# Kernel tuning notes

Measured on AMD Instinct MI355X. Metric: run time of the kernel, lower is better.

## Reference

```python
import jax, jax.numpy as jnp
import numpy as np

B, C, D, W, H = 4, 256, 32, 32, 32  # img_dim = D, in_channels = C, model_num = 4


def setup_inputs() -> dict:
    key = jax.random.key(0)
    ks = jax.random.split(key, 8)
    s = 0.02
    inp = {
        "m1": jax.random.normal(ks[0], (B, C, D, W, H), jnp.float32),
        "m2": jax.random.normal(ks[1], (B, C, D, W, H), jnp.float32),
        "m3": jax.random.normal(ks[2], (B, C, D, W, H), jnp.float32),
        "m4": jax.random.normal(ks[3], (B, C, D, W, H), jnp.float32),
        # nn.Linear weights (torch convention: y = x @ W.T + b)
        "Wq": jax.random.normal(ks[4], (D, D), jnp.float32) * s,
        "bq": jnp.zeros((D,), jnp.float32),
        "Wk": jax.random.normal(ks[5], (D, D), jnp.float32) * s,
        "bk": jnp.zeros((D,), jnp.float32),
        # four 1x1x1 Conv3d kernels, squeezed to [model, out_c, in_c]
        "Wc": jax.random.normal(ks[6], (4, C, C), jnp.float32) * s,
        "bc": jnp.zeros((4, C), jnp.float32),
    }
    return inp


def reference(m1, m2, m3, m4, Wq, bq, Wk, bk, Wc, bc):
    d = m1.shape[2]
    # adaptive_avg_pool3d(x, (D,1,1)) == mean over W,H -> [B,C,D]; stack 4 modalities -> [B,C,4,D]
    pooled = jnp.stack([m.mean(axis=(3, 4)) for m in (m1, m2, m3, m4)], axis=2)
    q = jnp.einsum('bcd,ed->bce', pooled[:, :, 0], Wq) + bq          # [B,C,D]
    k = jnp.einsum('bcmd,ed->bcme', pooled, Wk) + bk                 # [B,C,4,D]
    # per-modality attention logits: q . k_m over D -> [B,C,4]
    a = jnp.einsum('bcd,bcmd->bcm', q, k) / jnp.sqrt(jnp.float32(d))
    a = jax.nn.softmax(a, axis=-1)                                   # [B,C,4]
    ms = jnp.stack([m1, m2, m3, m4], axis=0)                         # [4,B,C,D,W,H]
    # 1x1x1 Conv3d == channel-mixing GEMM per voxel
    conv = jnp.einsum('mbcdwh,moc->mbodwh', ms, Wc) + bc[:, None, :, None, None, None]
    # weighted sum of the 4 conv outputs by per-(B,C) attention weights
    out = jnp.einsum('bcm,mbcdwh->bcdwh', a, conv)                   # [B,C,D,W,H]
    return out
```

## Files before the change

kernel.cpp:

```cpp
#include <hip/hip_runtime.h>
#include <hip/hip_bf16.h>

#define NB 4
#define NC 256
#define ND 32
#define WH 1024
#define DWH 32768
#define KTOT 1024

typedef __attribute__((ext_vector_type(8))) short short8;
typedef __attribute__((ext_vector_type(4))) float f32x4;

static __device__ __forceinline__ unsigned short f32_to_bf16(float f) {
    unsigned u = __builtin_bit_cast(unsigned, f);
    u = u + 0x7fff + ((u >> 16) & 1);
    return (unsigned short)(u >> 16);
}

static __device__ __forceinline__ unsigned pack_bf16x2(float lo, float hi) {
    __hip_bfloat162 h = __float22bfloat162_rn(make_float2(lo, hi));
    unsigned u;
    __builtin_memcpy(&u, &h, 4);
    return u;
}

__global__ __launch_bounds__(256) void transpool_kernel(
    const float* __restrict__ i0, const float* __restrict__ i1,
    const float* __restrict__ i2, const float* __restrict__ i3,
    unsigned short* __restrict__ Bt, float* __restrict__ pooled)
{
    __shared__ float lds[8 * 1024];
    int raw = blockIdx.x;
    int sb  = (raw & 7) * 2048 + (raw >> 3);
    int d    = sb & 31;
    int cb8  = (sb >> 5) & 31;
    int m    = (sb >> 10) & 3;
    int b    = sb >> 12;
    const float* base = (m == 0 ? i0 : m == 1 ? i1 : m == 2 ? i2 : i3)
                        + ((size_t)(b * NC + cb8 * 8)) * DWH + d * WH;

    int t = threadIdx.x;
    int row    = t >> 5;
    int lane32 = t & 31;

    float4 v[8];
    #pragma unroll
    for (int j = 0; j < 8; ++j)
        v[j] = *(const float4*)(base + (size_t)row * DWH + lane32 * 4 + j * 128);

    float s = 0.f;
    #pragma unroll
    for (int j = 0; j < 8; ++j)
        s += (v[j].x + v[j].y) + (v[j].z + v[j].w);

    #pragma unroll
    for (int j = 0; j < 8; ++j)
        *(float4*)&lds[row * 1024 + lane32 * 4 + j * 128] = v[j];
    __syncthreads();

    float4 c0 = *(const float4*)&lds[0 * 1024 + 4 * t];
    float4 c1 = *(const float4*)&lds[1 * 1024 + 4 * t];
    float4 c2 = *(const float4*)&lds[2 * 1024 + 4 * t];
    float4 c3 = *(const float4*)&lds[3 * 1024 + 4 * t];
    float4 c4 = *(const float4*)&lds[4 * 1024 + 4 * t];
    float4 c5 = *(const float4*)&lds[5 * 1024 + 4 * t];
    float4 c6 = *(const float4*)&lds[6 * 1024 + 4 * t];
    float4 c7 = *(const float4*)&lds[7 * 1024 + 4 * t];

    int kt = m * 4 + (cb8 >> 3);
    int kc = cb8 & 7;
    unsigned short* dst = Bt
        + ((((size_t)b * 16 + kt) * 8 + kc) * 32768 + (size_t)d * 1024 + 4 * t) * 8;
    const float* f0 = (const float*)&c0;  const float* f1 = (const float*)&c1;
    const float* f2 = (const float*)&c2;  const float* f3 = (const float*)&c3;
    const float* f4 = (const float*)&c4;  const float* f5 = (const float*)&c5;
    const float* f6 = (const float*)&c6;  const float* f7 = (const float*)&c7;
    #pragma unroll
    for (int xi = 0; xi < 4; ++xi) {
        uint4 pk = (uint4){pack_bf16x2(f0[xi], f1[xi]),
                           pack_bf16x2(f2[xi], f3[xi]),
                           pack_bf16x2(f4[xi], f5[xi]),
                           pack_bf16x2(f6[xi], f7[xi])};
        *(uint4*)(dst + xi * 8) = pk;
    }

    s += __shfl_down(s, 16, 64);
    s += __shfl_down(s, 8, 64);
    s += __shfl_down(s, 4, 64);
    s += __shfl_down(s, 2, 64);
    s += __shfl_down(s, 1, 64);
    if (lane32 == 0) {
        int c = cb8 * 8 + row;
        pooled[((size_t)b * NC + c) * 128 + m * 32 + d] = s * (1.0f / 1024.0f);
    }
}

__global__ __launch_bounds__(256) void pool_kernel(
    const float* __restrict__ i0, const float* __restrict__ i1,
    const float* __restrict__ i2, const float* __restrict__ i3,
    float* __restrict__ pooled)
{
    int bid = blockIdx.x;
    int m   = bid & 3;
    int bc  = bid >> 2;
    const float* src = (m == 0 ? i0 : m == 1 ? i1 : m == 2 ? i2 : i3)
                       + (size_t)bc * DWH;
    int t = threadIdx.x;
    int d   = t >> 3;
    int sub = t & 7;

    const float4* row = (const float4*)(src + (size_t)d * WH);
    float4 a0 = {0.f, 0.f, 0.f, 0.f}, a1 = {0.f, 0.f, 0.f, 0.f};
    #pragma unroll
    for (int j = 0; j < 16; ++j) {
        float4 u = row[sub + 8 * (2 * j)];
        float4 w = row[sub + 8 * (2 * j + 1)];
        a0.x += u.x; a0.y += u.y; a0.z += u.z; a0.w += u.w;
        a1.x += w.x; a1.y += w.y; a1.z += w.z; a1.w += w.w;
    }
    float s = (a0.x + a0.y) + (a0.z + a0.w) + (a1.x + a1.y) + (a1.z + a1.w);
    s += __shfl_down(s, 4, 64);
    s += __shfl_down(s, 2, 64);
    s += __shfl_down(s, 1, 64);
    if (sub == 0) pooled[bc * 128 + m * 32 + d] = s * (1.0f / 1024.0f);
}

__global__ __launch_bounds__(64) void attn_kernel(
    const float* __restrict__ pooled,
    const float* __restrict__ Wq, const float* __restrict__ bq,
    const float* __restrict__ Wk, const float* __restrict__ bk,
    const float* __restrict__ Wc, const float* __restrict__ bcv,
    unsigned short* __restrict__ Amat, float* __restrict__ beff)
{
    int bc_idx = blockIdx.x;
    int lane = threadIdx.x;
    int e = lane & 31;
    const float* P = pooled + bc_idx * 128;

    float q = 0.f, kv[4] = {0.f, 0.f, 0.f, 0.f};
    for (int d = 0; d < 32; ++d) {
        float pq = P[d];
        float wq = Wq[e * 32 + d], wk = Wk[e * 32 + d];
        q += pq * wq;
        #pragma unroll
        for (int m = 0; m < 4; ++m) kv[m] += P[m * 32 + d] * wk;
    }
    q += bq[e];
    #pragma unroll
    for (int m = 0; m < 4; ++m) kv[m] += bk[e];

    float lg[4];
    #pragma unroll
    for (int m = 0; m < 4; ++m) {
        float p = q * kv[m];
        #pragma unroll
        for (int off = 16; off; off >>= 1) p += __shfl_xor(p, off, 32);
        lg[m] = p * 0.17677669529663687f;
    }
    float mx = fmaxf(fmaxf(lg[0], lg[1]), fmaxf(lg[2], lg[3]));
    float ex[4], s = 0.f;
    #pragma unroll
    for (int m = 0; m < 4; ++m) { ex[m] = __expf(lg[m] - mx); s += ex[m]; }
    float a[4];
    #pragma unroll
    for (int m = 0; m < 4; ++m) a[m] = ex[m] / s;

    int c = bc_idx & 255;
    if (lane == 0) {
        float be = 0.f;
        #pragma unroll
        for (int m = 0; m < 4; ++m) be += a[m] * bcv[m * NC + c];
        beff[bc_idx] = be;
    }
    unsigned short* Arow = Amat + (size_t)bc_idx * KTOT;
    #pragma unroll
    for (int j = 0; j < 16; ++j) {
        int k = j * 64 + lane;
        int m = k >> 8, cin = k & 255;
        float v = a[m] * Wc[(m * NC + c) * NC + cin];
        Arow[k] = f32_to_bf16(v);
    }
}

#define BM 128
#define BN 128
#define BK 64

static __device__ __forceinline__ int swzA(int row, int chunk) {
    return row * 64 + ((chunk ^ (row & 7)) << 3);
}
static __device__ __forceinline__ int swzB(int row, int chunk) {
    return row * 64 + ((chunk ^ ((row >> 1) & 7)) << 3);
}

__global__ __launch_bounds__(256, 2) void gemm2_kernel(
    const unsigned short* __restrict__ Amat,
    const unsigned short* __restrict__ Bt,
    const float* __restrict__ beff,
    float* __restrict__ out)
{
    __shared__ __align__(16) short As[2 * BM * BK];
    __shared__ __align__(16) short Bs[2 * BN * BK];

    int raw = blockIdx.x;
    int sb  = (raw & 7) * 256 + (raw >> 3);
    int ot = sb & 1;
    int xt = (sb >> 1) & 255;
    int b  = sb >> 9;
    int o0 = ot * BM, x0 = xt * BN;

    int t = threadIdx.x;
    int wave = t >> 6, lane = t & 63;
    int wr = wave >> 1, wc = wave & 1;
    int lrow = lane & 15, lk = lane >> 4;
    int lr8 = lane >> 3;
    int aq  = (lane & 7) ^ lr8;

    const unsigned short* asrc = Amat + ((size_t)b * NC + o0) * KTOT
                                 + (size_t)(wave * 32 + lr8) * KTOT + aq * 8;
    const unsigned short* bsrc = Bt + (size_t)b * 16 * 2097152
                                 + (size_t)aq * 262144
                                 + ((size_t)xt * 128 + wave * 32 + lr8) * 8;

    f32x4 acc[4][4];
    #pragma unroll
    for (int mi = 0; mi < 4; ++mi)
        #pragma unroll
        for (int ni = 0; ni < 4; ++ni)
            acc[mi][ni] = (f32x4){0.f, 0.f, 0.f, 0.f};

    #pragma unroll
    for (int p = 0; p < 4; ++p)
        __builtin_amdgcn_global_load_lds(
            (const __attribute__((address_space(1))) unsigned int*)
                (asrc + (size_t)p * 8 * KTOT),
            (__attribute__((address_space(3))) unsigned int*)
                (As + (wave * 32 + p * 8) * 64), 16, 0, 0);
    #pragma unroll
    for (int p = 0; p < 4; ++p)
        __builtin_amdgcn_global_load_lds(
            (const __attribute__((address_space(1))) unsigned int*)
                (bsrc + (size_t)p * 64),
            (__attribute__((address_space(3))) unsigned int*)
                (Bs + (wave * 32 + p * 8) * 64), 16, 0, 0);
    __builtin_amdgcn_sched_barrier(0);

    #pragma unroll 1
    for (int it = 0; it < 16; ++it) {
        int ja = (it < 15) ? it + 1 : 15;
        int bo = ((it + 1) & 1) * (BM * BK);
        #pragma unroll
        for (int p = 0; p < 4; ++p)
            __builtin_amdgcn_global_load_lds(
                (const __attribute__((address_space(1))) unsigned int*)
                    (asrc + (size_t)p * 8 * KTOT + ja * BK),
                (__attribute__((address_space(3))) unsigned int*)
                    (As + bo + (wave * 32 + p * 8) * 64), 16, 0, 0);
        #pragma unroll
        for (int p = 0; p < 4; ++p)
            __builtin_amdgcn_global_load_lds(
                (const __attribute__((address_space(1))) unsigned int*)
                    (bsrc + (size_t)ja * 2097152 + p * 64),
                (__attribute__((address_space(3))) unsigned int*)
                    (Bs + bo + (wave * 32 + p * 8) * 64), 16, 0, 0);
        __builtin_amdgcn_sched_barrier(0);

        asm volatile("s_waitcnt vmcnt(8)" ::: "memory");
        __builtin_amdgcn_s_barrier();
        __builtin_amdgcn_sched_barrier(0);

        const short* Acur = As + (it & 1) * (BM * BK);
        const short* Bcur = Bs + (it & 1) * (BM * BK);
        #pragma unroll
        for (int kk = 0; kk < 2; ++kk) {
            int q = kk * 4 + lk;
            short8 af[4], bf[4];
            #pragma unroll
            for (int mi = 0; mi < 4; ++mi)
                af[mi] = *(const short8*)(&Acur[swzA(wr * 64 + mi * 16 + lrow, q)]);
            #pragma unroll
            for (int ni = 0; ni < 4; ++ni)
                bf[ni] = *(const short8*)(&Bcur[swzA(wc * 64 + ni * 16 + lrow, q)]);
            __builtin_amdgcn_s_setprio(1);
            #pragma unroll
            for (int mi = 0; mi < 4; ++mi)
                #pragma unroll
                for (int ni = 0; ni < 4; ++ni)
                    acc[mi][ni] = __builtin_amdgcn_mfma_f32_16x16x32_bf16(
                        af[mi], bf[ni], acc[mi][ni], 0, 0, 0);
            __builtin_amdgcn_s_setprio(0);
        }
        __builtin_amdgcn_s_barrier();
        __builtin_amdgcn_sched_barrier(0);
    }

    const float* beff_b = beff + b * NC + o0;
    float* outb = out + ((size_t)b * NC + o0) * DWH + x0;
    #pragma unroll
    for (int mi = 0; mi < 4; ++mi) {
        #pragma unroll
        for (int r4 = 0; r4 < 4; ++r4) {
            int row = wr * 64 + mi * 16 + lk * 4 + r4;
            float bias = beff_b[row];
            float* orow = outb + (size_t)row * DWH;
            #pragma unroll
            for (int ni = 0; ni < 4; ++ni) {
                int col = wc * 64 + ni * 16 + lrow;
                orow[col] = acc[mi][ni][r4] + bias;
            }
        }
    }
}

__global__ __launch_bounds__(256, 3) void gemm_kernel(
    const float* __restrict__ i0, const float* __restrict__ i1,
    const float* __restrict__ i2, const float* __restrict__ i3,
    const unsigned short* __restrict__ Amat,
    const float* __restrict__ beff,
    float* __restrict__ out)
{
    __shared__ __align__(16) short As[2 * BM * BK];
    __shared__ __align__(16) short Bs[BN * BK];

    int raw = blockIdx.x;
    int sb  = (raw & 7) * 256 + (raw >> 3);
    int ot = sb & 1;
    int xt = (sb >> 1) & 255;
    int b  = sb >> 9;
    int o0 = ot * BM, x0 = xt * BN;

    const unsigned short* Ab = Amat + ((size_t)b * NC + o0) * KTOT;

    int t = threadIdx.x;
    int wave = t >> 6, lane = t & 63;
    int wr = wave >> 1, wc = wave & 1;
    int lrow = lane & 15, lk = lane >> 4;

    f32x4 acc[4][4];
    #pragma unroll
    for (int mi = 0; mi < 4; ++mi)
        #pragma unroll
        for (int ni = 0; ni < 4; ++ni)
            acc[mi][ni] = (f32x4){0.f, 0.f, 0.f, 0.f};

    int xq = t & 31;
    int kb = (t >> 5) * 8;

    int ar = wave * 32 + (lane >> 3);
    int aq = (lane & 7) ^ (lane >> 3);
    const unsigned short* asrc = Ab + (size_t)ar * KTOT + aq * 8;

    float4 v[8];

    {
        #pragma unroll
        for (int p = 0; p < 4; ++p)
            __builtin_amdgcn_global_load_lds(
                (const __attribute__((address_space(1))) unsigned int*)
                    (asrc + (size_t)p * 8 * KTOT),
                (__attribute__((address_space(3))) unsigned int*)
                    (As + (wave * 32 + p * 8) * 64), 16, 0, 0);
        const float* Bb = i0 + (size_t)b * NC * DWH + x0;
        #pragma unroll
        for (int j = 0; j < 8; ++j)
            v[j] = *(const float4*)(Bb + (size_t)(kb + j) * DWH + xq * 4);
    }

    #pragma unroll 1
    for (int it = 0; it < KTOT / BK; ++it) {
        const short* Acur = As + (it & 1) * (BM * BK);
        short* Anx = As + ((it + 1) & 1) * (BM * BK);

        __builtin_amdgcn_s_barrier();
        __builtin_amdgcn_sched_barrier(0);

        {
            int ja = (it + 1 < 16) ? it + 1 : 15;
            #pragma unroll
            for (int p = 0; p < 4; ++p)
                __builtin_amdgcn_global_load_lds(
                    (const __attribute__((address_space(1))) unsigned int*)
                        (asrc + (size_t)p * 8 * KTOT + ja * BK),
                    (__attribute__((address_space(3))) unsigned int*)
                        (Anx + (wave * 32 + p * 8) * 64), 16, 0, 0);
        }
        __builtin_amdgcn_sched_barrier(0);

        uint4 pk[4];
        #pragma unroll
        for (int i = 0; i < 4; ++i) {
            unsigned w[4];
            #pragma unroll
            for (int j = 0; j < 4; ++j)
                w[j] = pack_bf16x2(((const float*)&v[2 * j])[i],
                                   ((const float*)&v[2 * j + 1])[i]);
            pk[i] = (uint4){w[0], w[1], w[2], w[3]};
        }

        {
            int itn = (it < 15) ? it + 1 : 15;
            int m = itn >> 2, cbase = (itn & 3) * 64;
            const float* Bb = (m == 0 ? i0 : m == 1 ? i1 : m == 2 ? i2 : i3)
                              + ((size_t)b * NC + cbase) * DWH + x0;
            #pragma unroll
            for (int j = 0; j < 8; ++j)
                v[j] = *(const float4*)(Bb + (size_t)(kb + j) * DWH + xq * 4);
        }
        __builtin_amdgcn_sched_barrier(0);

        #pragma unroll
        for (int i = 0; i < 4; ++i)
            *(uint4*)(&Bs[swzB(xq * 4 + i, t >> 5)]) = pk[i];

        asm volatile("s_waitcnt vmcnt(12) lgkmcnt(0)" ::: "memory");
        __builtin_amdgcn_s_barrier();
        __builtin_amdgcn_sched_barrier(0);

        #pragma unroll
        for (int kk = 0; kk < 2; ++kk) {
            int q = kk * 4 + lk;
            short8 af[4], bf[4];
            #pragma unroll
            for (int mi = 0; mi < 4; ++mi)
                af[mi] = *(const short8*)(&Acur[swzA(wr * 64 + mi * 16 + lrow, q)]);
            #pragma unroll
            for (int ni = 0; ni < 4; ++ni)
                bf[ni] = *(const short8*)(&Bs[swzB(wc * 64 + ni * 16 + lrow, q)]);
            __builtin_amdgcn_s_setprio(1);
            #pragma unroll
            for (int mi = 0; mi < 4; ++mi)
                #pragma unroll
                for (int ni = 0; ni < 4; ++ni)
                    acc[mi][ni] = __builtin_amdgcn_mfma_f32_16x16x32_bf16(
                        af[mi], bf[ni], acc[mi][ni], 0, 0, 0);
            __builtin_amdgcn_s_setprio(0);
        }
    }

    const float* beff_b = beff + b * NC + o0;
    float* outb = out + ((size_t)b * NC + o0) * DWH + x0;
    #pragma unroll
    for (int mi = 0; mi < 4; ++mi) {
        #pragma unroll
        for (int r4 = 0; r4 < 4; ++r4) {
            int row = wr * 64 + mi * 16 + lk * 4 + r4;
            float bias = beff_b[row];
            float* orow = outb + (size_t)row * DWH;
            #pragma unroll
            for (int ni = 0; ni < 4; ++ni) {
                int col = wc * 64 + ni * 16 + lrow;
                orow[col] = acc[mi][ni][r4] + bias;
            }
        }
    }
}

extern "C" void kernel_launch(void* const* d_in, const int* in_sizes, int n_in,
                              void* d_out, int out_size, void* d_ws, size_t ws_size,
                              hipStream_t stream) {
    const float* m1 = (const float*)d_in[0];
    const float* m2 = (const float*)d_in[1];
    const float* m3 = (const float*)d_in[2];
    const float* m4 = (const float*)d_in[3];
    const float* Wq = (const float*)d_in[4];
    const float* bq = (const float*)d_in[5];
    const float* Wk = (const float*)d_in[6];
    const float* bk = (const float*)d_in[7];
    const float* Wc = (const float*)d_in[8];
    const float* bcv = (const float*)d_in[9];
    float* out = (float*)d_out;

    const size_t BT_BYTES = (size_t)NB * KTOT * DWH * 2;
    const size_t NEED = BT_BYTES + 524288 + 2097152 + 4096;

    if (ws_size >= NEED) {
        unsigned short* Btr   = (unsigned short*)d_ws;
        float* pooled         = (float*)((char*)d_ws + BT_BYTES);
        unsigned short* Amat  = (unsigned short*)((char*)d_ws + BT_BYTES + 524288);
        float* beff           = (float*)((char*)d_ws + BT_BYTES + 524288 + 2097152);

        transpool_kernel<<<16384, 256, 0, stream>>>(m1, m2, m3, m4, Btr, pooled);
        attn_kernel<<<NB * NC, 64, 0, stream>>>(pooled, Wq, bq, Wk, bk, Wc, bcv,
                                                Amat, beff);
        gemm2_kernel<<<2048, 256, 0, stream>>>(Amat, Btr, beff, out);
    } else {
        float* pooled        = (float*)d_ws;
        unsigned short* Amat = (unsigned short*)((char*)d_ws + 524288);
        float* beff          = (float*)((char*)d_ws + 524288 + 2097152);

        pool_kernel<<<NB * NC * 4, 256, 0, stream>>>(m1, m2, m3, m4, pooled);
        attn_kernel<<<NB * NC, 64, 0, stream>>>(pooled, Wq, bq, Wk, bk, Wc, bcv,
                                                Amat, beff);
        gemm_kernel<<<(NB) * (NC / BM) * (DWH / BN), 256, 0, stream>>>(
            m1, m2, m3, m4, Amat, beff, out);
    }
}
```

Before: 294.9 us.

## Make transpose-pool kernel persistent over 8 depth slices with register double buffering

The transpose/pool kernel now has each block process 8 consecutive depth slices instead of one, and the grid shrinks from 16384 to 2048 blocks. Loads for the next slice go into a second register buffer while the current slice is written through LDS, converted to bf16 and stored, so global reads overlap the LDS transpose. This is meant to hide memory latency and cut per-block launch overhead. It roughly doubles register use, which may lower occupancy, and adds two barriers per slice.

New measurement: 305.0 us. 3.4% more time.

```diff
diff --git a/kernel.cpp b/kernel.cpp
--- a/kernel.cpp
+++ b/kernel.cpp
@@ -23,6 +23,55 @@
     __builtin_memcpy(&u, &h, 4);
     return u;
 }
+
+#define TP_LOAD(V, J)                                                         \
+  { const float* bs_ = base + (size_t)(J) * WH;                               \
+    _Pragma("unroll")                                                         \
+    for (int j_ = 0; j_ < 8; ++j_)                                            \
+      V[j_] = *(const float4*)(bs_ + (size_t)row * DWH + lane32 * 4 + j_ * 128); }
+
+#define TP_ITEM(VC, VN, J)                                                    \
+  {                                                                           \
+    _Pragma("unroll")                                                         \
+    for (int j_ = 0; j_ < 8; ++j_)                                            \
+      *(float4*)&lds[row * 1024 + lane32 * 4 + j_ * 128] = VC[j_];            \
+    if ((J) + 1 < 8) { TP_LOAD(VN, (J) + 1); }                                \
+    asm volatile("s_waitcnt lgkmcnt(0)" ::: "memory");                        \
+    __builtin_amdgcn_s_barrier();                                             \
+    __builtin_amdgcn_sched_barrier(0);                                        \
+    {                                                                         \
+      float4 c_[8];                                                           \
+      _Pragma("unroll")                                                       \
+      for (int ci_ = 0; ci_ < 8; ++ci_)                                       \
+        c_[ci_] = *(const float4*)&lds[ci_ * 1024 + 4 * t];                   \
+      unsigned short* dst_ = dstbase + (size_t)(d0 + (J)) * 8192 + (size_t)t * 32; \
+      _Pragma("unroll")                                                       \
+      for (int xi_ = 0; xi_ < 4; ++xi_) {                                     \
+        uint4 pk_ = (uint4){                                                  \
+          pack_bf16x2(((const float*)&c_[0])[xi_], ((const float*)&c_[1])[xi_]), \
+          pack_bf16x2(((const float*)&c_[2])[xi_], ((const float*)&c_[3])[xi_]), \
+          pack_bf16x2(((const float*)&c_[4])[xi_], ((const float*)&c_[5])[xi_]), \
+          pack_bf16x2(((const float*)&c_[6])[xi_], ((const float*)&c_[7])[xi_])};\
+        *(uint4*)(dst_ + xi_ * 8) = pk_;                                      \
+      }                                                                       \
+    }                                                                         \
+    {                                                                         \
+      float s_ = 0.f;                                                         \
+      _Pragma("unroll")                                                       \
+      for (int j_ = 0; j_ < 8; ++j_)                                          \
+        s_ += (VC[j_].x + VC[j_].y) + (VC[j_].z + VC[j_].w);                  \
+      s_ += __shfl_down(s_, 16, 64);                                          \
+      s_ += __shfl_down(s_, 8, 64);                                           \
+      s_ += __shfl_down(s_, 4, 64);                                           \
+      s_ += __shfl_down(s_, 2, 64);                                           \
+      s_ += __shfl_down(s_, 1, 64);                                           \
+      if (lane32 == 0)                                                        \
+        pooled[((size_t)b * NC + cb8 * 8 + row) * 128 + m * 32 + d0 + (J)]    \
+            = s_ * (1.0f / 1024.0f);                                          \
+    }                                                                         \
+    __builtin_amdgcn_s_barrier();                                             \
+    __builtin_amdgcn_sched_barrier(0);                                        \
+  }
 
 __global__ __launch_bounds__(256) void transpool_kernel(
     const float* __restrict__ i0, const float* __restrict__ i1,
@@ -31,67 +80,29 @@
 {
     __shared__ float lds[8 * 1024];
     int raw = blockIdx.x;
-    int sb  = (raw & 7) * 2048 + (raw >> 3);
-    int d    = sb & 31;
-    int cb8  = (sb >> 5) & 31;
-    int m    = (sb >> 10) & 3;
-    int b    = sb >> 12;
+    int sp  = (raw & 7) * 256 + (raw >> 3);
+    int d0   = (sp & 3) * 8;
+    int cb8  = (sp >> 2) & 31;
+    int m    = (sp >> 7) & 3;
+    int b    = sp >> 9;
     const float* base = (m == 0 ? i0 : m == 1 ? i1 : m == 2 ? i2 : i3)
-                        + ((size_t)(b * NC + cb8 * 8)) * DWH + d * WH;
+                        + ((size_t)(b * NC + cb8 * 8)) * DWH + d0 * WH;
 
     int t = threadIdx.x;
     int row    = t >> 5;
     int lane32 = t & 31;
 
-    float4 v[8];
-    #pragma unroll
-    for (int j = 0; j < 8; ++j)
-        v[j] = *(const float4*)(base + (size_t)row * DWH + lane32 * 4 + j * 128);
-
-    float s = 0.f;
-    #pragma unroll
-    for (int j = 0; j < 8; ++j)
-        s += (v[j].x + v[j].y) + (v[j].z + v[j].w);
-
-    #pragma unroll
-    for (int j = 0; j < 8; ++j)
-        *(float4*)&lds[row * 1024 + lane32 * 4 + j * 128] = v[j];
-    __syncthreads();
-
-    float4 c0 = *(const float4*)&lds[0 * 1024 + 4 * t];
-    float4 c1 = *(const float4*)&lds[1 * 1024 + 4 * t];
-    float4 c2 = *(const float4*)&lds[2 * 1024 + 4 * t];
-    float4 c3 = *(const float4*)&lds[3 * 1024 + 4 * t];
-    float4 c4 = *(const float4*)&lds[4 * 1024 + 4 * t];
-    float4 c5 = *(const float4*)&lds[5 * 1024 + 4 * t];
-    float4 c6 = *(const float4*)&lds[6 * 1024 + 4 * t];
-    float4 c7 = *(const float4*)&lds[7 * 1024 + 4 * t];
-
     int kt = m * 4 + (cb8 >> 3);
     int kc = cb8 & 7;
-    unsigned short* dst = Bt
-        + ((((size_t)b * 16 + kt) * 8 + kc) * 32768 + (size_t)d * 1024 + 4 * t) * 8;
-    const float* f0 = (const float*)&c0;  const float* f1 = (const float*)&c1;
-    const float* f2 = (const float*)&c2;  const float* f3 = (const float*)&c3;
-    const float* f4 = (const float*)&c4;  const float* f5 = (const float*)&c5;
-    const float* f6 = (const float*)&c6;  const float* f7 = (const float*)&c7;
-    #pragma unroll
-    for (int xi = 0; xi < 4; ++xi) {
-        uint4 pk = (uint4){pack_bf16x2(f0[xi], f1[xi]),
-                           pack_bf16x2(f2[xi], f3[xi]),
-                           pack_bf16x2(f4[xi], f5[xi]),
-                           pack_bf16x2(f6[xi], f7[xi])};
-        *(uint4*)(dst + xi * 8) = pk;
-    }
-
-    s += __shfl_down(s, 16, 64);
-    s += __shfl_down(s, 8, 64);
-    s += __shfl_down(s, 4, 64);
-    s += __shfl_down(s, 2, 64);
-    s += __shfl_down(s, 1, 64);
-    if (lane32 == 0) {
-        int c = cb8 * 8 + row;
-        pooled[((size_t)b * NC + c) * 128 + m * 32 + d] = s * (1.0f / 1024.0f);
+    unsigned short* dstbase = Bt + (((size_t)b * 16 + kt) * 8 + kc) * 262144;
+
+    float4 va[8], vb[8];
+    TP_LOAD(va, 0);
+
+    #pragma unroll 1
+    for (int j2 = 0; j2 < 4; ++j2) {
+        TP_ITEM(va, vb, 2 * j2);
+        TP_ITEM(vb, va, 2 * j2 + 1);
     }
 }
 
@@ -479,7 +490,7 @@
         unsigned short* Amat  = (unsigned short*)((char*)d_ws + BT_BYTES + 524288);
         float* beff           = (float*)((char*)d_ws + BT_BYTES + 524288 + 2097152);
 
-        transpool_kernel<<<16384, 256, 0, stream>>>(m1, m2, m3, m4, Btr, pooled);
+        transpool_kernel<<<2048, 256, 0, stream>>>(m1, m2, m3, m4, Btr, pooled);
         attn_kernel<<<NB * NC, 64, 0, stream>>>(pooled, Wq, bq, Wk, bk, Wc, bcv,
                                                 Amat, beff);
         gemm2_kernel<<<2048, 256, 0, stream>>>(Amat, Btr, beff, out);
```
